# Performance work log

Measured on AMD Instinct MI355X. Metric: run time of the kernel, lower is better.

Reference implementation:

```python
import jax, jax.numpy as jnp
import numpy as np

BS, L, SRC, E, H = 8, 1024, 1024, 768, 12
D = E // H  # head dim = 64


def setup_inputs() -> dict:
    key = jax.random.key(0)
    ks = jax.random.split(key, 12)
    p = lambda k, shp: (jax.random.normal(k, shp, jnp.float32) * 0.02)
    return {
        "query": jax.random.normal(ks[0], (BS, L, E), jnp.float32),
        "key": jax.random.normal(ks[1], (BS, SRC, E), jnp.float32),
        "value": jax.random.normal(ks[2], (BS, SRC, E), jnp.float32),
        "key_padding_mask": jax.random.uniform(ks[3], (BS, SRC), jnp.float32),
        "Wq": p(ks[4], (E, E)), "bq": jnp.zeros((E,), jnp.float32),
        "Wk": p(ks[5], (E, E)), "bk": jnp.zeros((E,), jnp.float32),
        "Wv": p(ks[6], (E, E)), "bv": jnp.zeros((E,), jnp.float32),
        "Wo": p(ks[7], (E, E)), "bo": jnp.zeros((E,), jnp.float32),
        "scaling_factors": jnp.array([-64, -64, -64, -32, -32, -32, -16, -16, -16, -8, -8, -8], jnp.float32),
    }


def reference(query, key, value, key_padding_mask, Wq, bq, Wk, bk, Wv, bv, Wo, bo, scaling_factors):
    bs = query.shape[0]
    # projections (torch Linear: x @ W.T + b)
    q = query @ Wq.T + bq          # [bs, L, E]
    k = key @ Wk.T + bk            # [bs, S, E]
    v = value @ Wv.T + bv          # [bs, S, E]
    # split heads
    q = q.reshape(bs, -1, H, D).transpose(0, 2, 1, 3)  # [bs, H, L, D]
    k = k.reshape(bs, -1, H, D).transpose(0, 2, 1, 3)  # [bs, H, S, D]
    v = v.reshape(bs, -1, H, D).transpose(0, 2, 1, 3)  # [bs, H, S, D]
    q = q / jnp.sqrt(jnp.float32(D))
    scores = jnp.einsum("bhld,bhsd->bhls", q, k)       # [bs, H, L, S]
    # soft key-padding bias: kpm[b,s] * scaling_factors[h]
    bias = key_padding_mask[:, None, None, :] * scaling_factors[None, :, None, None]
    scores = scores + bias
    attn = jax.nn.softmax(scores, axis=-1)             # dropout p=0 (eval)
    out = jnp.einsum("bhls,bhsd->bhld", attn, v)       # [bs, H, L, D]
    out = out.transpose(0, 2, 1, 3).reshape(bs, -1, E)  # [bs, L, E]
    return out @ Wo.T + bo
```

## Files before the change

### kernel.cpp

```cpp
#include <hip/hip_runtime.h>
#include <hip/hip_bf16.h>

typedef __attribute__((ext_vector_type(8))) short bf16x8;
typedef __attribute__((ext_vector_type(4))) short bf16x4;
typedef __attribute__((ext_vector_type(4))) float f32x4;

#define H_BS 8
#define H_L 1024
#define H_S 1024
#define H_E 768
#define H_NH 12
#define H_HD 64
#define EE (H_E * H_E)
#define AN (H_BS * H_L * H_E)
#define LOG2E 1.44269504f

static __device__ __forceinline__ short cvtbf(float f) {
  __hip_bfloat16 h = __float2bfloat16(f);
  return *reinterpret_cast<short*>(&h);
}

static __device__ __forceinline__ float fexp2(float x) {
#if __has_builtin(__builtin_amdgcn_exp2f)
  return __builtin_amdgcn_exp2f(x);
#else
  return __expf(x * 0.69314718056f);
#endif
}

static __device__ __forceinline__ void gload16(const void* g, void* l) {
  __builtin_amdgcn_global_load_lds(
      (const __attribute__((address_space(1))) void*)g,
      (__attribute__((address_space(3))) void*)l, 16, 0, 0);
}

__global__ __launch_bounds__(256)
void conv_bf16(const float* __restrict__ w0, const float* __restrict__ w1,
               const float* __restrict__ w2, const float* __restrict__ w3,
               const float* __restrict__ a0, const float* __restrict__ a1,
               const float* __restrict__ a2,
               short* __restrict__ ws_w, short* __restrict__ ws_a)
{
  const int y = blockIdx.y;
  const float* src;
  short* dst;
  int n;
  if (y < 4) {
    src = (y == 0) ? w0 : (y == 1) ? w1 : (y == 2) ? w2 : w3;
    dst = ws_w + (size_t)y * EE;
    n = EE;
  } else {
    src = (y == 4) ? a0 : (y == 5) ? a1 : a2;
    dst = ws_a + (size_t)(y - 4) * AN;
    n = AN;
  }
  const int i = (blockIdx.x * 256 + threadIdx.x) * 8;
  if (i >= n) return;
  const float4 f0 = *reinterpret_cast<const float4*>(src + i);
  const float4 f1 = *reinterpret_cast<const float4*>(src + i + 4);
  bf16x8 r;
  r[0] = cvtbf(f0.x); r[1] = cvtbf(f0.y); r[2] = cvtbf(f0.z); r[3] = cvtbf(f0.w);
  r[4] = cvtbf(f1.x); r[5] = cvtbf(f1.y); r[6] = cvtbf(f1.z); r[7] = cvtbf(f1.w);
  *reinterpret_cast<bf16x8*>(dst + i) = r;
}

__global__ __launch_bounds__(256)
void qkv_gemm(const short* __restrict__ Abf, const short* __restrict__ Wbf,
              const float* __restrict__ bq, const float* __restrict__ bk,
              const float* __restrict__ bv, short* __restrict__ oq,
              short* __restrict__ ok_, short* __restrict__ ov)
{
  __shared__ short a_s[128][32];
  __shared__ short w_s[128][32];

  const int mode = blockIdx.z;
  const short* A = Abf + (size_t)mode * AN;
  const short* W = Wbf + (size_t)mode * EE;
  const float* bias = (mode == 0) ? bq : (mode == 1) ? bk : bv;

  const int m0 = blockIdx.y * 128;
  const int n0 = blockIdx.x * 128;
  const int t = threadIdx.x;
  const int lane = t & 63;
  const int wv = t >> 6;
  const int wr = wv >> 1;
  const int wc = wv & 1;
  const int lr = lane & 15;
  const int lg = lane >> 4;

  f32x4 acc[4][4];
  const f32x4 zero = {0.f, 0.f, 0.f, 0.f};
  #pragma unroll
  for (int i = 0; i < 4; ++i)
    #pragma unroll
    for (int j = 0; j < 4; ++j) acc[i][j] = zero;

  const int g0 = wv * 2;
  const int srow = lane >> 2;
  const int scol = (lane & 3) * 8;
  const short* aptr0 = A + (size_t)(m0 + g0 * 16 + srow) * H_E + scol;
  const short* aptr1 = aptr0 + 16 * H_E;
  const short* wptr0 = W + (size_t)(n0 + g0 * 16 + srow) * H_E + scol;
  const short* wptr1 = wptr0 + 16 * H_E;
  short* adst0 = &a_s[0][0] + g0 * 512;
  short* adst1 = adst0 + 512;
  short* wdst0 = &w_s[0][0] + g0 * 512;
  short* wdst1 = wdst0 + 512;

  for (int kt = 0; kt < H_E / 32; ++kt) {
    const int ko = kt * 32;
    __syncthreads();
    gload16(aptr0 + ko, adst0);
    gload16(aptr1 + ko, adst1);
    gload16(wptr0 + ko, wdst0);
    gload16(wptr1 + ko, wdst1);
    __syncthreads();
    bf16x8 af[4], wf[4];
    #pragma unroll
    for (int i = 0; i < 4; ++i)
      af[i] = *reinterpret_cast<const bf16x8*>(&a_s[wr * 64 + i * 16 + lr][lg * 8]);
    #pragma unroll
    for (int j = 0; j < 4; ++j)
      wf[j] = *reinterpret_cast<const bf16x8*>(&w_s[wc * 64 + j * 16 + lr][lg * 8]);
    #pragma unroll
    for (int i = 0; i < 4; ++i)
      #pragma unroll
      for (int j = 0; j < 4; ++j)
        acc[i][j] = __builtin_amdgcn_mfma_f32_16x16x32_bf16(af[i], wf[j], acc[i][j], 0, 0, 0);
  }

  #pragma unroll
  for (int j = 0; j < 4; ++j) {
    const int gn = n0 + wc * 64 + j * 16 + lr;
    const float bvl = bias[gn];
    const int hh = gn >> 6, dd = gn & 63;
    #pragma unroll
    for (int i = 0; i < 4; ++i) {
      #pragma unroll
      for (int e = 0; e < 4; ++e) {
        const int gm = m0 + wr * 64 + i * 16 + lg * 4 + e;
        const float val = acc[i][j][e] + bvl;
        const int bb = gm >> 10, ll = gm & 1023;
        if (mode == 0)
          oq[((size_t)(bb * H_NH + hh) * H_L + ll) * H_HD + dd] = cvtbf(val * (0.125f * LOG2E));
        else if (mode == 1)
          ok_[((size_t)(bb * H_NH + hh) * H_S + ll) * H_HD + dd] = cvtbf(val);
        else
          ov[((size_t)(bb * H_NH + hh) * H_HD + dd) * H_S + ll] = cvtbf(val);
      }
    }
  }
}

__global__ __launch_bounds__(256)
void out_gemm(const short* __restrict__ A, const short* __restrict__ W,
              const float* __restrict__ bias, float* __restrict__ outp)
{
  __shared__ short a_s[128][32];
  __shared__ short w_s[128][32];

  const int m0 = blockIdx.y * 128;
  const int n0 = blockIdx.x * 128;
  const int t = threadIdx.x;
  const int lane = t & 63;
  const int wv = t >> 6;
  const int wr = wv >> 1;
  const int wc = wv & 1;
  const int lr = lane & 15;
  const int lg = lane >> 4;

  f32x4 acc[4][4];
  const f32x4 zero = {0.f, 0.f, 0.f, 0.f};
  #pragma unroll
  for (int i = 0; i < 4; ++i)
    #pragma unroll
    for (int j = 0; j < 4; ++j) acc[i][j] = zero;

  const int g0 = wv * 2;
  const int srow = lane >> 2;
  const int scol = (lane & 3) * 8;
  const short* aptr0 = A + (size_t)(m0 + g0 * 16 + srow) * H_E + scol;
  const short* aptr1 = aptr0 + 16 * H_E;
  const short* wptr0 = W + (size_t)(n0 + g0 * 16 + srow) * H_E + scol;
  const short* wptr1 = wptr0 + 16 * H_E;
  short* adst0 = &a_s[0][0] + g0 * 512;
  short* adst1 = adst0 + 512;
  short* wdst0 = &w_s[0][0] + g0 * 512;
  short* wdst1 = wdst0 + 512;

  for (int kt = 0; kt < H_E / 32; ++kt) {
    const int ko = kt * 32;
    __syncthreads();
    gload16(aptr0 + ko, adst0);
    gload16(aptr1 + ko, adst1);
    gload16(wptr0 + ko, wdst0);
    gload16(wptr1 + ko, wdst1);
    __syncthreads();
    bf16x8 af[4], wf[4];
    #pragma unroll
    for (int i = 0; i < 4; ++i)
      af[i] = *reinterpret_cast<const bf16x8*>(&a_s[wr * 64 + i * 16 + lr][lg * 8]);
    #pragma unroll
    for (int j = 0; j < 4; ++j)
      wf[j] = *reinterpret_cast<const bf16x8*>(&w_s[wc * 64 + j * 16 + lr][lg * 8]);
    #pragma unroll
    for (int i = 0; i < 4; ++i)
      #pragma unroll
      for (int j = 0; j < 4; ++j)
        acc[i][j] = __builtin_amdgcn_mfma_f32_16x16x32_bf16(af[i], wf[j], acc[i][j], 0, 0, 0);
  }

  #pragma unroll
  for (int j = 0; j < 4; ++j) {
    const int gn = n0 + wc * 64 + j * 16 + lr;
    const float bvl = bias[gn];
    #pragma unroll
    for (int i = 0; i < 4; ++i) {
      #pragma unroll
      for (int e = 0; e < 4; ++e) {
        const int gm = m0 + wr * 64 + i * 16 + lg * 4 + e;
        outp[(size_t)gm * H_E + gn] = acc[i][j][e] + bvl;
      }
    }
  }
}

__global__ __launch_bounds__(256)
void smha_attn(const short* __restrict__ q, const short* __restrict__ k,
               const short* __restrict__ vt, const float* __restrict__ kpm,
               const float* __restrict__ sf, short* __restrict__ outp)
{
  __shared__ short k_s[64][72];
  __shared__ short v_s[64][72];
  __shared__ short p_s[4][16][72];

  const int blk = blockIdx.x;
  const int qt = blk & 15;
  const int hh = (blk >> 4) % H_NH;
  const int bb = blk / (16 * H_NH);
  const int bh = bb * H_NH + hh;
  const int t = threadIdx.x;
  const int wv = t >> 6;
  const int lane = t & 63;
  const int lr = lane & 15;
  const int lg = lane >> 4;

  const int q0 = qt * 64 + wv * 16;

  bf16x8 qf[2];
  #pragma unroll
  for (int kk = 0; kk < 2; ++kk)
    qf[kk] = *reinterpret_cast<const bf16x8*>(
        &q[((size_t)bh * H_L + q0 + lr) * H_HD + kk * 32 + lg * 8]);

  const float sfh = sf[hh] * LOG2E;
  const float* kpmb = kpm + bb * H_S;

  f32x4 o_acc[4];
  const f32x4 zero = {0.f, 0.f, 0.f, 0.f};
  #pragma unroll
  for (int di = 0; di < 4; ++di) o_acc[di] = zero;
  float mrow = -1e30f, lrow = 0.f;

  const int srow = t >> 2;
  const int scol = (t & 3) * 16;

  const short* kp = &k[((size_t)bh * H_S + srow) * H_HD + scol];
  const short* vp = &vt[((size_t)bh * H_HD + srow) * H_S + scol];
  bf16x8 kr0 = *reinterpret_cast<const bf16x8*>(kp);
  bf16x8 kr1 = *reinterpret_cast<const bf16x8*>(kp + 8);
  bf16x8 vr0 = *reinterpret_cast<const bf16x8*>(vp);
  bf16x8 vr1 = *reinterpret_cast<const bf16x8*>(vp + 8);

  for (int kv = 0; kv < H_S / 64; ++kv) {
    const int s0 = kv * 64;
    __syncthreads();
    *reinterpret_cast<bf16x8*>(&k_s[srow][scol])     = kr0;
    *reinterpret_cast<bf16x8*>(&k_s[srow][scol + 8]) = kr1;
    *reinterpret_cast<bf16x8*>(&v_s[srow][scol])     = vr0;
    *reinterpret_cast<bf16x8*>(&v_s[srow][scol + 8]) = vr1;
    __syncthreads();
    if (kv + 1 < H_S / 64) {
      const short* kpn = kp + (size_t)(kv + 1) * 64 * H_HD;
      const short* vpn = vp + (size_t)(kv + 1) * 64;
      kr0 = *reinterpret_cast<const bf16x8*>(kpn);
      kr1 = *reinterpret_cast<const bf16x8*>(kpn + 8);
      vr0 = *reinterpret_cast<const bf16x8*>(vpn);
      vr1 = *reinterpret_cast<const bf16x8*>(vpn + 8);
    }

    f32x4 sc[4];
    #pragma unroll
    for (int ni = 0; ni < 4; ++ni) {
      const f32x4 kp4 = *reinterpret_cast<const f32x4*>(&kpmb[s0 + ni * 16 + lg * 4]);
      #pragma unroll
      for (int e = 0; e < 4; ++e) sc[ni][e] = kp4[e] * sfh;
    }
    #pragma unroll
    for (int kk = 0; kk < 2; ++kk) {
      #pragma unroll
      for (int ni = 0; ni < 4; ++ni) {
        const bf16x8 kf = *reinterpret_cast<const bf16x8*>(&k_s[ni * 16 + lr][kk * 32 + lg * 8]);
        sc[ni] = __builtin_amdgcn_mfma_f32_16x16x32_bf16(kf, qf[kk], sc[ni], 0, 0, 0);
      }
    }

    float pm[4];
    #pragma unroll
    for (int ni = 0; ni < 4; ++ni)
      pm[ni] = fmaxf(fmaxf(sc[ni][0], sc[ni][1]), fmaxf(sc[ni][2], sc[ni][3]));
    float mx = fmaxf(fmaxf(pm[0], pm[1]), fmaxf(pm[2], pm[3]));
    mx = fmaxf(mx, __shfl_xor(mx, 16));
    mx = fmaxf(mx, __shfl_xor(mx, 32));

    if (!__all(mx <= mrow + 11.5f)) {
      const float mnew = fmaxf(mrow, mx);
      const float scal = fexp2(mrow - mnew);
      lrow *= scal;
      float sj[4];
      #pragma unroll
      for (int j = 0; j < 4; ++j) sj[j] = __shfl(scal, lg * 4 + j);
      #pragma unroll
      for (int di = 0; di < 4; ++di)
        #pragma unroll
        for (int j = 0; j < 4; ++j) o_acc[di][j] *= sj[j];
      mrow = mnew;
    }

    float ps[4];
    #pragma unroll
    for (int ni = 0; ni < 4; ++ni) {
      #pragma unroll
      for (int e = 0; e < 4; ++e) sc[ni][e] = fexp2(sc[ni][e] - mrow);
      ps[ni] = (sc[ni][0] + sc[ni][1]) + (sc[ni][2] + sc[ni][3]);
    }
    float rs = (ps[0] + ps[1]) + (ps[2] + ps[3]);
    rs += __shfl_xor(rs, 16);
    rs += __shfl_xor(rs, 32);
    lrow += rs;

    #pragma unroll
    for (int ni = 0; ni < 4; ++ni) {
      bf16x4 pk4;
      pk4[0] = cvtbf(sc[ni][0]); pk4[1] = cvtbf(sc[ni][1]);
      pk4[2] = cvtbf(sc[ni][2]); pk4[3] = cvtbf(sc[ni][3]);
      *reinterpret_cast<bf16x4*>(&p_s[wv][lr][ni * 16 + lg * 4]) = pk4;
    }

    #pragma unroll
    for (int kk = 0; kk < 2; ++kk) {
      const bf16x8 pf = *reinterpret_cast<const bf16x8*>(&p_s[wv][lr][kk * 32 + lg * 8]);
      #pragma unroll
      for (int di = 0; di < 4; ++di) {
        const bf16x8 vfr = *reinterpret_cast<const bf16x8*>(&v_s[di * 16 + lr][kk * 32 + lg * 8]);
        o_acc[di] = __builtin_amdgcn_mfma_f32_16x16x32_bf16(pf, vfr, o_acc[di], 0, 0, 0);
      }
    }
  }

  #pragma unroll
  for (int j = 0; j < 4; ++j) {
    const float rl = 1.0f / __shfl(lrow, lg * 4 + j);
    const int gq = q0 + lg * 4 + j;
    #pragma unroll
    for (int di = 0; di < 4; ++di)
      outp[((size_t)bb * H_L + gq) * H_E + hh * H_HD + di * 16 + lr] =
          cvtbf(o_acc[di][j] * rl);
  }
}

extern "C" void kernel_launch(void* const* d_in, const int* in_sizes, int n_in,
                              void* d_out, int out_size, void* d_ws, size_t ws_size,
                              hipStream_t stream)
{
  short* ws_w  = (short*)d_ws;
  short* ws_a  = ws_w + (size_t)4 * EE;
  short* ws_q  = ws_a + (size_t)3 * AN;
  short* ws_k  = ws_q + AN;
  short* ws_vt = ws_k + AN;
  short* ws_at = ws_a;

  conv_bf16<<<dim3(AN / 2048, 7), 256, 0, stream>>>(
      (const float*)d_in[4], (const float*)d_in[6], (const float*)d_in[8],
      (const float*)d_in[10], (const float*)d_in[0], (const float*)d_in[1],
      (const float*)d_in[2], ws_w, ws_a);

  qkv_gemm<<<dim3(H_E / 128, (H_BS * H_L) / 128, 3), 256, 0, stream>>>(
      ws_a, ws_w, (const float*)d_in[5], (const float*)d_in[7],
      (const float*)d_in[9], ws_q, ws_k, ws_vt);

  smha_attn<<<H_BS * H_NH * (H_L / 64), 256, 0, stream>>>(
      ws_q, ws_k, ws_vt, (const float*)d_in[3], (const float*)d_in[12], ws_at);

  out_gemm<<<dim3(H_E / 128, (H_BS * H_L) / 128), 256, 0, stream>>>(
      ws_at, ws_w + (size_t)3 * EE, (const float*)d_in[11], (float*)d_out);
}
```

Baseline: 290.0 us.

## Double-buffer GEMM LDS loads, stage transposed V stores, prioritize attention MFMAs

Both projection GEMMs now double-buffer the LDS tiles, issuing the next K-slice's async global-to-LDS loads before computing the current one. This overlaps memory latency with MFMA work and drops one barrier per iteration. The V projection epilogue stages the tile transposed in LDS (padded rows) so the transposed V layout is written with 16-byte coalesced stores instead of scattered 2-byte stores. The attention kernel raises wave priority around its MFMA blocks with s_setprio. The cost is doubled LDS per block, which may lower occupancy.

```diff
diff --git a/kernel.cpp b/kernel.cpp
--- a/kernel.cpp
+++ b/kernel.cpp
@@ -14,6 +14,7 @@
 #define EE (H_E * H_E)
 #define AN (H_BS * H_L * H_E)
 #define LOG2E 1.44269504f
+#define NKT (H_E / 32)
 
 static __device__ __forceinline__ short cvtbf(float f) {
   __hip_bfloat16 h = __float2bfloat16(f);
@@ -70,8 +71,7 @@
               const float* __restrict__ bv, short* __restrict__ oq,
               short* __restrict__ ok_, short* __restrict__ ov)
 {
-  __shared__ short a_s[128][32];
-  __shared__ short w_s[128][32];
+  __shared__ short smem[16896];
 
   const int mode = blockIdx.z;
   const short* A = Abf + (size_t)mode * AN;
@@ -102,51 +102,87 @@
   const short* aptr1 = aptr0 + 16 * H_E;
   const short* wptr0 = W + (size_t)(n0 + g0 * 16 + srow) * H_E + scol;
   const short* wptr1 = wptr0 + 16 * H_E;
-  short* adst0 = &a_s[0][0] + g0 * 512;
-  short* adst1 = adst0 + 512;
-  short* wdst0 = &w_s[0][0] + g0 * 512;
-  short* wdst1 = wdst0 + 512;
-
-  for (int kt = 0; kt < H_E / 32; ++kt) {
-    const int ko = kt * 32;
-    __syncthreads();
-    gload16(aptr0 + ko, adst0);
-    gload16(aptr1 + ko, adst1);
-    gload16(wptr0 + ko, wdst0);
-    gload16(wptr1 + ko, wdst1);
-    __syncthreads();
+
+  {
+    short* b = smem;
+    gload16(aptr0, b + g0 * 512);
+    gload16(aptr1, b + g0 * 512 + 512);
+    gload16(wptr0, b + 4096 + g0 * 512);
+    gload16(wptr1, b + 4096 + g0 * 512 + 512);
+  }
+  __syncthreads();
+
+  int cur = 0;
+  for (int kt = 0; kt < NKT; ++kt) {
+    if (kt + 1 < NKT) {
+      const int ko = (kt + 1) * 32;
+      short* b = smem + (cur ^ 1) * 8192;
+      gload16(aptr0 + ko, b + g0 * 512);
+      gload16(aptr1 + ko, b + g0 * 512 + 512);
+      gload16(wptr0 + ko, b + 4096 + g0 * 512);
+      gload16(wptr1 + ko, b + 4096 + g0 * 512 + 512);
+    }
+    const short* ab = smem + cur * 8192;
+    const short* wb = ab + 4096;
     bf16x8 af[4], wf[4];
     #pragma unroll
     for (int i = 0; i < 4; ++i)
-      af[i] = *reinterpret_cast<const bf16x8*>(&a_s[wr * 64 + i * 16 + lr][lg * 8]);
+      af[i] = *reinterpret_cast<const bf16x8*>(&ab[(wr * 64 + i * 16 + lr) * 32 + lg * 8]);
     #pragma unroll
     for (int j = 0; j < 4; ++j)
-      wf[j] = *reinterpret_cast<const bf16x8*>(&w_s[wc * 64 + j * 16 + lr][lg * 8]);
+      wf[j] = *reinterpret_cast<const bf16x8*>(&wb[(wc * 64 + j * 16 + lr) * 32 + lg * 8]);
     #pragma unroll
     for (int i = 0; i < 4; ++i)
       #pragma unroll
       for (int j = 0; j < 4; ++j)
         acc[i][j] = __builtin_amdgcn_mfma_f32_16x16x32_bf16(af[i], wf[j], acc[i][j], 0, 0, 0);
-  }
-
-  #pragma unroll
-  for (int j = 0; j < 4; ++j) {
-    const int gn = n0 + wc * 64 + j * 16 + lr;
-    const float bvl = bias[gn];
-    const int hh = gn >> 6, dd = gn & 63;
-    #pragma unroll
-    for (int i = 0; i < 4; ++i) {
-      #pragma unroll
-      for (int e = 0; e < 4; ++e) {
-        const int gm = m0 + wr * 64 + i * 16 + lg * 4 + e;
-        const float val = acc[i][j][e] + bvl;
-        const int bb = gm >> 10, ll = gm & 1023;
-        if (mode == 0)
-          oq[((size_t)(bb * H_NH + hh) * H_L + ll) * H_HD + dd] = cvtbf(val * (0.125f * LOG2E));
-        else if (mode == 1)
-          ok_[((size_t)(bb * H_NH + hh) * H_S + ll) * H_HD + dd] = cvtbf(val);
-        else
-          ov[((size_t)(bb * H_NH + hh) * H_HD + dd) * H_S + ll] = cvtbf(val);
+    __syncthreads();
+    cur ^= 1;
+  }
+
+  if (mode == 2) {
+    #pragma unroll
+    for (int j = 0; j < 4; ++j) {
+      const int gnl = wc * 64 + j * 16 + lr;
+      const float bvl = bias[n0 + gnl];
+      #pragma unroll
+      for (int i = 0; i < 4; ++i) {
+        bf16x4 pk;
+        #pragma unroll
+        for (int e = 0; e < 4; ++e) pk[e] = cvtbf(acc[i][j][e] + bvl);
+        *reinterpret_cast<bf16x4*>(&smem[gnl * 132 + wr * 64 + i * 16 + lg * 4]) = pk;
+      }
+    }
+    __syncthreads();
+    const int bb = m0 >> 10;
+    const int lbase = m0 & 1023;
+    #pragma unroll
+    for (int u = 0; u < 8; ++u) {
+      const int gnl = wv * 32 + u * 4 + lg;
+      const int gn = n0 + gnl;
+      const int hh = gn >> 6, dd = gn & 63;
+      const bf16x8 vvv = *reinterpret_cast<const bf16x8*>(&smem[gnl * 132 + lr * 8]);
+      *reinterpret_cast<bf16x8*>(
+          &ov[((size_t)(bb * H_NH + hh) * H_HD + dd) * H_S + lbase + lr * 8]) = vvv;
+    }
+  } else {
+    #pragma unroll
+    for (int j = 0; j < 4; ++j) {
+      const int gn = n0 + wc * 64 + j * 16 + lr;
+      const float bvl = bias[gn];
+      const int hh = gn >> 6, dd = gn & 63;
+      #pragma unroll
+      for (int i = 0; i < 4; ++i) {
+        #pragma unroll
+        for (int e = 0; e < 4; ++e) {
+          const int gm = m0 + wr * 64 + i * 16 + lg * 4 + e;
+          const float val = acc[i][j][e] + bvl;
+          const int bb = gm >> 10, ll = gm & 1023;
+          if (mode == 0)
+            oq[((size_t)(bb * H_NH + hh) * H_L + ll) * H_HD + dd] = cvtbf(val * (0.125f * LOG2E));
+          else
+            ok_[((size_t)(bb * H_NH + hh) * H_S + ll) * H_HD + dd] = cvtbf(val);
+        }
       }
     }
   }
@@ -156,8 +192,7 @@
 void out_gemm(const short* __restrict__ A, const short* __restrict__ W,
               const float* __restrict__ bias, float* __restrict__ outp)
 {
-  __shared__ short a_s[128][32];
-  __shared__ short w_s[128][32];
+  __shared__ short smem[16384];
 
   const int m0 = blockIdx.y * 128;
   const int n0 = blockIdx.x * 128;
@@ -183,31 +218,42 @@
   const short* aptr1 = aptr0 + 16 * H_E;
   const short* wptr0 = W + (size_t)(n0 + g0 * 16 + srow) * H_E + scol;
   const short* wptr1 = wptr0 + 16 * H_E;
-  short* adst0 = &a_s[0][0] + g0 * 512;
-  short* adst1 = adst0 + 512;
-  short* wdst0 = &w_s[0][0] + g0 * 512;
-  short* wdst1 = wdst0 + 512;
-
-  for (int kt = 0; kt < H_E / 32; ++kt) {
-    const int ko = kt * 32;
-    __syncthreads();
-    gload16(aptr0 + ko, adst0);
-    gload16(aptr1 + ko, adst1);
-    gload16(wptr0 + ko, wdst0);
-    gload16(wptr1 + ko, wdst1);
-    __syncthreads();
+
+  {
+    short* b = smem;
+    gload16(aptr0, b + g0 * 512);
+    gload16(aptr1, b + g0 * 512 + 512);
+    gload16(wptr0, b + 4096 + g0 * 512);
+    gload16(wptr1, b + 4096 + g0 * 512 + 512);
+  }
+  __syncthreads();
+
+  int cur = 0;
+  for (int kt = 0; kt < NKT; ++kt) {
+    if (kt + 1 < NKT) {
+      const int ko = (kt + 1) * 32;
+      short* b = smem + (cur ^ 1) * 8192;
+      gload16(aptr0 + ko, b + g0 * 512);
+      gload16(aptr1 + ko, b + g0 * 512 + 512);
+      gload16(wptr0 + ko, b + 4096 + g0 * 512);
+      gload16(wptr1 + ko, b + 4096 + g0 * 512 + 512);
+    }
+    const short* ab = smem + cur * 8192;
+    const short* wb = ab + 4096;
     bf16x8 af[4], wf[4];
     #pragma unroll
     for (int i = 0; i < 4; ++i)
-      af[i] = *reinterpret_cast<const bf16x8*>(&a_s[wr * 64 + i * 16 + lr][lg * 8]);
+      af[i] = *reinterpret_cast<const bf16x8*>(&ab[(wr * 64 + i * 16 + lr) * 32 + lg * 8]);
     #pragma unroll
     for (int j = 0; j < 4; ++j)
-      wf[j] = *reinterpret_cast<const bf16x8*>(&w_s[wc * 64 + j * 16 + lr][lg * 8]);
+      wf[j] = *reinterpret_cast<const bf16x8*>(&wb[(wc * 64 + j * 16 + lr) * 32 + lg * 8]);
     #pragma unroll
     for (int i = 0; i < 4; ++i)
       #pragma unroll
       for (int j = 0; j < 4; ++j)
         acc[i][j] = __builtin_amdgcn_mfma_f32_16x16x32_bf16(af[i], wf[j], acc[i][j], 0, 0, 0);
+    __syncthreads();
+    cur ^= 1;
   }
 
   #pragma unroll
@@ -296,6 +342,7 @@
       #pragma unroll
       for (int e = 0; e < 4; ++e) sc[ni][e] = kp4[e] * sfh;
     }
+    __builtin_amdgcn_s_setprio(1);
     #pragma unroll
     for (int kk = 0; kk < 2; ++kk) {
       #pragma unroll
@@ -304,6 +351,7 @@
         sc[ni] = __builtin_amdgcn_mfma_f32_16x16x32_bf16(kf, qf[kk], sc[ni], 0, 0, 0);
       }
     }
+    __builtin_amdgcn_s_setprio(0);
 
     float pm[4];
     #pragma unroll
@@ -347,6 +395,7 @@
       *reinterpret_cast<bf16x4*>(&p_s[wv][lr][ni * 16 + lg * 4]) = pk4;
     }
 
+    __builtin_amdgcn_s_setprio(1);
     #pragma unroll
     for (int kk = 0; kk < 2; ++kk) {
       const bf16x8 pf = *reinterpret_cast<const bf16x8*>(&p_s[wv][lr][kk * 32 + lg * 8]);
@@ -356,6 +405,7 @@
         o_acc[di] = __builtin_amdgcn_mfma_f32_16x16x32_bf16(pf, vfr, o_acc[di], 0, 0, 0);
       }
     }
+    __builtin_amdgcn_s_setprio(0);
   }
 
   #pragma unroll
```

Result: faster. 271.7 us (-6.3%).
